# Kernel tuning notes

Measured on AMD Instinct MI355X. Metric: run time of the kernel, lower is better.

The kernel has to match this reference:

```python
import jax, jax.numpy as jnp
import numpy as np

C_IN = 144
PC = 288           # proj_channels = 2 * in_channels
HEADS = 12
DG = 12            # deformable groups
CLIP = 2
KH = KW = 3
A = KH * KW        # samples per clip per group (attention window 3x3)
PAD = 1
MAXMAG = 10.0
B, T, H, W = 1, 1, 64, 64


def _conv2d(x, w, b, pad):
    y = jax.lax.conv_general_dilated(x, w, (1, 1), [(pad, pad), (pad, pad)],
                                     dimension_numbers=('NCHW', 'OIHW', 'NCHW'))
    return y + b[None, :, None, None]


def _lrelu(x):
    return jnp.where(x >= 0, x, 0.1 * x)


def _linear_c(x, w, b):
    # per-pixel linear on channel dim; x: (..., Cin, h, w), w: (Cin, Cout)
    return jnp.einsum('...ihw,io->...ohw', x, w) + b[:, None, None]


def _bilinear_gather(feat, py, px):
    # feat: (b, clip, g, cg, h, w); py/px: (b, clip, g, A, h, w) absolute pixel coords
    # zero padding outside image (deformable-conv sampling semantics)
    b, cl, g, cg, h, w = feat.shape
    ff = feat.reshape(b, cl, g, cg, h * w)
    y0 = jnp.floor(py)
    x0 = jnp.floor(px)
    wy1 = py - y0
    wx1 = px - x0

    def corner(yc, xc, wt):
        valid = ((yc >= 0) & (yc < h) & (xc >= 0) & (xc < w)).astype(feat.dtype)
        yi = jnp.clip(yc, 0, h - 1).astype(jnp.int32)
        xi = jnp.clip(xc, 0, w - 1).astype(jnp.int32)
        idx = (yi * w + xi).reshape(b, cl, g, 1, -1)
        gat = jnp.take_along_axis(ff, idx, axis=-1).reshape(b, cl, g, cg, *py.shape[3:])
        return gat * (wt * valid)[:, :, :, None]

    out = corner(y0, x0, (1 - wy1) * (1 - wx1))
    out = out + corner(y0, x0 + 1, (1 - wy1) * wx1)
    out = out + corner(y0 + 1, x0, wy1 * (1 - wx1))
    out = out + corner(y0 + 1, x0 + 1, wy1 * wx1)
    return out  # (b, clip, g, cg, A, h, w)


def setup_inputs() -> dict:
    key = jax.random.key(0)
    ks = jax.random.split(key, 32)
    rn = lambda i, shp, s=1.0: jax.random.normal(ks[i], shp, dtype=jnp.float32) * s
    cin_off = C_IN * (1 + CLIP) + CLIP * 2   # 436
    c_off = CLIP * DG * A * 2                # 432
    d = {
        'q': rn(0, (B, T, C_IN, H, W)),
        'k': rn(1, (B, CLIP, C_IN, H, W)),
        'v': rn(2, (B, CLIP, C_IN, H, W)),
        'vpw0': rn(3, (B, T, C_IN, H, W)),
        'vpw1': rn(4, (B, T, C_IN, H, W)),
        'flow0': rn(5, (B, T, 2, H, W), 3.0),
        'flow1': rn(6, (B, T, 2, H, W), 3.0),
        'wo1': rn(7, (64, cin_off, 1, 1), 1.0 / np.sqrt(cin_off)),
        'bo1': rn(8, (64,), 0.01),
        'wo2': rn(9, (64, 64, 3, 3), 1.0 / np.sqrt(64 * 9)),
        'bo2': rn(10, (64,), 0.01),
        'wo3': rn(11, (64, 64, 3, 3), 1.0 / np.sqrt(64 * 9)),
        'bo3': rn(12, (64,), 0.01),
        'wo4': rn(13, (64, 64, 3, 3), 1.0 / np.sqrt(64 * 9)),
        'bo4': rn(14, (64,), 0.01),
        'wo5': rn(15, (64, 64, 3, 3), 1.0 / np.sqrt(64 * 9)),
        'bo5': rn(16, (64,), 0.01),
        'wo6': rn(17, (c_off, 64, 1, 1), 0.02),
        'bo6': rn(18, (c_off,), 0.01),
        'wq': rn(19, (C_IN, PC), 1.0 / np.sqrt(C_IN)),
        'bq': rn(20, (PC,), 0.01),
        'wk': rn(21, (C_IN, PC), 1.0 / np.sqrt(C_IN)),
        'bk': rn(22, (PC,), 0.01),
        'wv': rn(23, (C_IN, PC), 1.0 / np.sqrt(C_IN)),
        'bv': rn(24, (PC,), 0.01),
        'wp': rn(25, (PC, C_IN), 1.0 / np.sqrt(PC)),
        'bp': rn(26, (C_IN,), 0.01),
        'wm1': rn(27, (C_IN, 2 * C_IN), 1.0 / np.sqrt(C_IN)),
        'bm1': rn(28, (2 * C_IN,), 0.01),
        'wm2': rn(29, (2 * C_IN, C_IN), 1.0 / np.sqrt(2 * C_IN)),
        'bm2': rn(30, (C_IN,), 0.01),
    }
    return d


def reference(q, k, v, vpw0, vpw1, flow0, flow1,
              wo1, bo1, wo2, bo2, wo3, bo3, wo4, bo4, wo5, bo5, wo6, bo6,
              wq, bq, wk, bk, wv, bv, wp, bp, wm1, bm1, wm2, bm2):
    b, t, c, h, w = q.shape  # t == 1 here so q batch b*t matches kv batch b
    bt = b * t
    # --- offset predictor: Conv3d stack with time-kernel 1 == 2D convs ---
    x = jnp.concatenate([q, vpw0, vpw1, flow0, flow1], axis=2).reshape(bt, -1, h, w)
    x = _lrelu(_conv2d(x, wo1, bo1, 0))
    x = _lrelu(_conv2d(x, wo2, bo2, 1))
    x = _lrelu(_conv2d(x, wo3, bo3, 1))
    x = _lrelu(_conv2d(x, wo4, bo4, 1))
    x = _lrelu(_conv2d(x, wo5, bo5, 1))
    off = MAXMAG * jnp.tanh(_conv2d(x, wo6, bo6, 0))  # (bt, CLIP*DG*A*2, h, w)
    # add optical flow (channel-flipped to (y, x)) to every sample offset
    fyx = flow0.reshape(bt, 2, h, w)[:, ::-1]
    off = off + jnp.tile(fyx, (1, off.shape[1] // 2, 1, 1))
    off = off.reshape(bt, CLIP, DG, A, 2, h, w)
    ar = jnp.arange(A)
    by = (ar // KW - PAD).astype(q.dtype)  # kernel base offsets (stride=1, dil=1)
    bx = (ar % KW - PAD).astype(q.dtype)
    py = off[:, :, :, :, 0] + by[None, None, None, :, None, None] \
         + jnp.arange(h, dtype=q.dtype)[:, None]
    px = off[:, :, :, :, 1] + bx[None, None, None, :, None, None] \
         + jnp.arange(w, dtype=q.dtype)
    # --- q/k/v projections ---
    hd = PC // HEADS
    qp = _linear_c(q, wq, bq).reshape(bt, HEADS, hd, h, w)
    kp = _linear_c(k, wk, bk).reshape(b, CLIP, DG, PC // DG, h, w)
    vp = _linear_c(v, wv, bv).reshape(b, CLIP, DG, PC // DG, h, w)
    # --- deformable bilinear gather (per deformable group) ---
    ksamp = _bilinear_gather(kp, py, px).reshape(bt, CLIP, HEADS, hd, A, h, w)
    vsamp = _bilinear_gather(vp, py, px).reshape(bt, CLIP, HEADS, hd, A, h, w)
    # --- attention over CLIP*A sampled locations, per pixel per head ---
    scores = jnp.einsum('bmdyx,bcmdayx->bmcayx', qp, ksamp) * (hd ** -0.5)
    attn = jax.nn.softmax(scores.reshape(bt, HEADS, CLIP * A, h, w), axis=2)
    vflat = vsamp.transpose(0, 2, 1, 4, 3, 5, 6).reshape(bt, HEADS, CLIP * A, hd, h, w)
    out = jnp.einsum('bmsyx,bmsdyx->bmdyx', attn, vflat).reshape(b, t, PC, h, w)
    # --- output projection + MLP residual ---
    o = _linear_c(out, wp, bp)
    m = _linear_c(jax.nn.gelu(_linear_c(o, wm1, bm1), approximate=False), wm2, bm2)
    return o + m
```

## Files before the change

kernel.cpp:

```cpp
#include <hip/hip_runtime.h>
#include <hip/hip_bf16.h>
#include <math.h>

typedef __hip_bfloat16 bf16;
typedef __attribute__((ext_vector_type(8))) short bf16x8v;
typedef __attribute__((ext_vector_type(4))) float f32x4v;

#define NPIX 4096

__device__ __forceinline__ float b2f(bf16 v) { return __bfloat162float(v); }
__device__ __forceinline__ unsigned short f2bu(float f) {
    bf16 h = __float2bfloat16(f);
    return *(unsigned short*)&h;
}
__device__ __forceinline__ int detect_bf16(const unsigned short* __restrict__ qraw) {
    int lane = threadIdx.x & 63;
    unsigned short u = qraw[lane * 2];
    int e = (u >> 7) & 0xFF;
    unsigned long long ball = __ballot(e >= 100 && e <= 135);
    return __popcll(ball) > 32;
}
__device__ __forceinline__ float rdval(const void* s, int idx, int isbf) {
    return isbf ? b2f(((const bf16*)s)[idx]) : ((const float*)s)[idx];
}

#define OF_WO6 175680
#define OF_BO6 203328
#define OF_BO1 27904
#define OF_BO2 64832
#define OF_BO3 101760
#define OF_BO4 138688
#define OF_BO5 175616
#define OF_BQ  245232
#define OF_BK  286992
#define OF_BV  328752
#define OF_BP  370512
#define OF_BM1 412128
#define OF_BM2 453888
#define OF_FL0 454032

struct CArgs { const void* src[14]; int dstoff[14]; int n[14]; };
struct PPJob { const void* src; int dstS; int Mp, Kp, kr, mr, sstride, kind; };
struct PPArgs { PPJob j[11]; };

__global__ void misc_kernel(CArgs a, PPArgs pa, const void* __restrict__ q,
                            const void* __restrict__ k, const void* __restrict__ v,
                            const void* __restrict__ vp0, const void* __restrict__ vp1,
                            const void* __restrict__ fl0, const void* __restrict__ fl1,
                            float* __restrict__ cw, short* __restrict__ XS,
                            short* __restrict__ X1, short* __restrict__ wsS)
{
    const int isbf = detect_bf16((const unsigned short*)q);
    const int y = blockIdx.y;
    if (y < 14) {
        const int n = a.n[y];
        float* d = cw + a.dstoff[y];
        if (isbf) {
            const bf16* s = (const bf16*)a.src[y];
            for (int i = blockIdx.x * 256 + threadIdx.x; i < n; i += 256 * 16) d[i] = b2f(s[i]);
        } else {
            const float* s = (const float*)a.src[y];
            for (int i = blockIdx.x * 256 + threadIdx.x; i < n; i += 256 * 16) d[i] = s[i];
        }
    } else if (y < 24) {
        const int job = y - 14;
        const int z = job >> 1, half = job & 1;
        const int p = blockIdx.x * 256 + threadIdx.x;
        const void* srcs[5] = { q, k, k, v, v };
        const int clips[5] = { 0, 0, 1, 0, 1 };
        const size_t co = (size_t)clips[z] * 144 * NPIX;
        short* row = XS + (size_t)z * 655360 + (size_t)p * 160;
        for (int c0 = half * 72; c0 < half * 72 + 72; c0 += 8) {
            unsigned short h[8];
            if (isbf) {
                const bf16* s = (const bf16*)srcs[z] + co;
#pragma unroll
                for (int i = 0; i < 8; ++i) h[i] = f2bu(b2f(s[(size_t)(c0 + i) * NPIX + p]));
            } else {
                const float* s = (const float*)srcs[z] + co;
#pragma unroll
                for (int i = 0; i < 8; ++i) h[i] = f2bu(s[(size_t)(c0 + i) * NPIX + p]);
            }
            uint4 u;
            u.x = (unsigned)h[0] | ((unsigned)h[1] << 16);
            u.y = (unsigned)h[2] | ((unsigned)h[3] << 16);
            u.z = (unsigned)h[4] | ((unsigned)h[5] << 16);
            u.w = (unsigned)h[6] | ((unsigned)h[7] << 16);
            *(uint4*)(row + c0) = u;
        }
        if (half == 1) {
            uint4 zz; zz.x = zz.y = zz.z = zz.w = 0u;
            *(uint4*)(row + 144) = zz;
            *(uint4*)(row + 152) = zz;
        }
    } else if (y < 28) {
        const int sec = y - 24;
        const int p = blockIdx.x * 256 + threadIdx.x;
        short* row = X1 + (size_t)p * 448;
        if (sec < 3) {
            const void* srcs[3] = { q, vp0, vp1 };
            const int cbase = sec * 144;
            for (int c0 = 0; c0 < 144; c0 += 8) {
                unsigned short h[8];
                if (isbf) {
                    const bf16* s = (const bf16*)srcs[sec];
#pragma unroll
                    for (int i = 0; i < 8; ++i) h[i] = f2bu(b2f(s[(size_t)(c0 + i) * NPIX + p]));
                } else {
                    const float* s = (const float*)srcs[sec];
#pragma unroll
                    for (int i = 0; i < 8; ++i) h[i] = f2bu(s[(size_t)(c0 + i) * NPIX + p]);
                }
                uint4 u;
                u.x = (unsigned)h[0] | ((unsigned)h[1] << 16);
                u.y = (unsigned)h[2] | ((unsigned)h[3] << 16);
                u.z = (unsigned)h[4] | ((unsigned)h[5] << 16);
                u.w = (unsigned)h[6] | ((unsigned)h[7] << 16);
                *(uint4*)(row + cbase + c0) = u;
            }
        } else {
            unsigned short h[4];
            if (isbf) {
                const bf16* f0 = (const bf16*)fl0;
                const bf16* f1 = (const bf16*)fl1;
                h[0] = f2bu(b2f(f0[p]));
                h[1] = f2bu(b2f(f0[NPIX + p]));
                h[2] = f2bu(b2f(f1[p]));
                h[3] = f2bu(b2f(f1[NPIX + p]));
            } else {
                const float* f0 = (const float*)fl0;
                const float* f1 = (const float*)fl1;
                h[0] = f2bu(f0[p]);
                h[1] = f2bu(f0[NPIX + p]);
                h[2] = f2bu(f1[p]);
                h[3] = f2bu(f1[NPIX + p]);
            }
            uint4 u;
            u.x = (unsigned)h[0] | ((unsigned)h[1] << 16);
            u.y = (unsigned)h[2] | ((unsigned)h[3] << 16);
            u.z = 0u; u.w = 0u;
            *(uint4*)(row + 432) = u;
            uint4 zz; zz.x = zz.y = zz.z = zz.w = 0u;
            *(uint4*)(row + 440) = zz;
        }
    } else {
        PPJob J = pa.j[y - 28];
        const int tot = J.Mp * J.Kp;
        for (int e = blockIdx.x * 256 + threadIdx.x; e < tot; e += 256 * 16) {
            int m = e / J.Kp, kk = e - m * J.Kp;
            float vv = 0.f;
            if (J.kind == 0) { if (kk < J.kr) vv = rdval(J.src, m * J.sstride + kk, isbf); }
            else if (J.kind == 1) { if (kk < J.kr && m < J.mr) vv = rdval(J.src, kk * J.sstride + m, isbf); }
            else { int c = kk & 63, tap = kk >> 6; if (kk < J.kr) vv = rdval(J.src, m * J.sstride + c * 9 + tap, isbf); }
            wsS[J.dstS + e] = (short)f2bu(vv);
        }
    }
}

struct GemmDesc {
    const short* A; const short* B; const float* bias;
    void* dst; void* dst2; const unsigned short* qraw;
    int Mp, Mreal, mode, gofs, ostride, obase, nwaves;
};
struct GemmDesc5 { GemmDesc d[5]; };

template <int TM, int TN, int BM, int KP>
__global__ __launch_bounds__(256) void gemm_kernel(GemmDesc5 gd)
{
    const GemmDesc d = gd.d[blockIdx.z];
    const int wid = blockIdx.x * 4 + (threadIdx.x >> 6);
    if (wid >= d.nwaves) return;
    const int lane = threadIdx.x & 63;
    const int tiles_m = d.Mp / (16 * TM);
    const int m0 = (wid % tiles_m) * (16 * TM);
    const int p0 = (wid / tiles_m) * (16 * TN);
    const int ar = lane & 15;
    const int kq = (lane >> 4) * 8;

    f32x4v acc[TM][TN];
#pragma unroll
    for (int i = 0; i < TM; ++i)
#pragma unroll
        for (int j = 0; j < TN; ++j) acc[i][j] = (f32x4v){0.f, 0.f, 0.f, 0.f};

#pragma unroll
    for (int k0 = 0; k0 < KP; k0 += 32) {
        bf16x8v a[TM], b[TN];
#pragma unroll
        for (int i = 0; i < TM; ++i)
            a[i] = *(const bf16x8v*)(d.A + (size_t)(m0 + i * 16 + ar) * KP + k0 + kq);
        if (BM == 0) {
#pragma unroll
            for (int j = 0; j < TN; ++j)
                b[j] = *(const bf16x8v*)(d.B + (size_t)(p0 + j * 16 + ar) * KP + k0 + kq);
        } else {
            const int tap = k0 >> 6;
            const int cc = (k0 & 63) + kq;
            const int dy = tap / 3 - 1, dx = tap % 3 - 1;
#pragma unroll
            for (int j = 0; j < TN; ++j) {
                const int pix = p0 + j * 16 + ar;
                const int yy = (pix >> 6) + dy, xx = (pix & 63) + dx;
                const bool ok = ((unsigned)yy < 64u) & ((unsigned)xx < 64u);
                const int np = min(max(yy, 0), 63) * 64 + min(max(xx, 0), 63);
                bf16x8v bv = *(const bf16x8v*)(d.B + (size_t)np * 64 + cc);
                if (!ok) bv = (bf16x8v)(short)0;
                b[j] = bv;
            }
        }
#pragma unroll
        for (int i = 0; i < TM; ++i)
#pragma unroll
            for (int j = 0; j < TN; ++j)
                acc[i][j] = __builtin_amdgcn_mfma_f32_16x16x32_bf16(a[i], b[j], acc[i][j], 0, 0, 0);
    }

    const int isbf = (d.mode == 5) ? detect_bf16(d.qraw) : 0;
#pragma unroll
    for (int i = 0; i < TM; ++i) {
#pragma unroll
        for (int j = 0; j < TN; ++j) {
            const int pcol = p0 + j * 16 + (lane & 15);
            const int mb = m0 + i * 16 + (lane >> 4) * 4;
            float vv[4];
#pragma unroll
            for (int r = 0; r < 4; ++r) {
                const int m = mb + r;
                vv[r] = acc[i][j][r];
                if (m < d.Mreal) vv[r] += d.bias[m];
            }
            if (d.mode == 0) {
#pragma unroll
                for (int r = 0; r < 4; ++r) vv[r] = (vv[r] >= 0.f) ? vv[r] : 0.1f * vv[r];
                uint2 u;
                u.x = (unsigned)f2bu(vv[0]) | ((unsigned)f2bu(vv[1]) << 16);
                u.y = (unsigned)f2bu(vv[2]) | ((unsigned)f2bu(vv[3]) << 16);
                *(uint2*)((unsigned short*)d.dst + (size_t)pcol * d.Mp + mb) = u;
            } else if (d.mode == 1) {
                const int g = mb / 24 + d.gofs;
                uint2 u;
                u.x = (unsigned)f2bu(vv[0]) | ((unsigned)f2bu(vv[1]) << 16);
                u.y = (unsigned)f2bu(vv[2]) | ((unsigned)f2bu(vv[3]) << 16);
                *(uint2*)((unsigned short*)d.dst +
                          ((size_t)g * NPIX + pcol) * d.ostride + (mb % 24) + d.obase) = u;
            } else if (d.mode == 3) {
                uint2 u;
                u.x = (unsigned)f2bu(vv[0]) | ((unsigned)f2bu(vv[1]) << 16);
                u.y = (unsigned)f2bu(vv[2]) | ((unsigned)f2bu(vv[3]) << 16);
                *(uint2*)((unsigned short*)d.dst + (size_t)pcol * 160 + mb) = u;
                if (mb < 144)
                    *(float4*)((float*)d.dst2 + (size_t)pcol * 144 + mb) =
                        make_float4(vv[0], vv[1], vv[2], vv[3]);
            } else if (d.mode == 4) {
#pragma unroll
                for (int r = 0; r < 4; ++r)
                    vv[r] = 0.5f * vv[r] * (1.f + erff(vv[r] * 0.70710678118654752f));
                uint2 u;
                u.x = (unsigned)f2bu(vv[0]) | ((unsigned)f2bu(vv[1]) << 16);
                u.y = (unsigned)f2bu(vv[2]) | ((unsigned)f2bu(vv[3]) << 16);
                *(uint2*)((unsigned short*)d.dst + (size_t)pcol * d.Mp + mb) = u;
            } else {
#pragma unroll
                for (int r = 0; r < 4; ++r) {
                    const int m = mb + r;
                    if (m < 144) {
                        float v = vv[r] + ((float*)d.dst2)[(size_t)pcol * 144 + m];
                        if (isbf) ((unsigned short*)d.dst)[(size_t)m * NPIX + pcol] = f2bu(v);
                        else      ((float*)d.dst)[(size_t)m * NPIX + pcol] = v;
                    }
                }
            }
        }
    }
}

__global__ __launch_bounds__(256) void conv6_kernel(const short* __restrict__ YF,
                                                    const float* __restrict__ cw,
                                                    float* __restrict__ py, float* __restrict__ px)
{
    const int p = blockIdx.x * 256 + threadIdx.x;
    const int o0 = blockIdx.y * 16;
    const uint4* yrow = (const uint4*)(YF + (size_t)p * 64);
    const float* wb = cw + OF_WO6 + o0 * 64;

    float acc[16];
#pragma unroll
    for (int j = 0; j < 16; ++j) acc[j] = cw[OF_BO6 + o0 + j];

#pragma unroll
    for (int c = 0; c < 8; ++c) {
        uint4 u = yrow[c];
        float a0 = __uint_as_float(u.x << 16);
        float a1 = __uint_as_float(u.x & 0xFFFF0000u);
        float a2 = __uint_as_float(u.y << 16);
        float a3 = __uint_as_float(u.y & 0xFFFF0000u);
        float a4 = __uint_as_float(u.z << 16);
        float a5 = __uint_as_float(u.z & 0xFFFF0000u);
        float a6 = __uint_as_float(u.w << 16);
        float a7 = __uint_as_float(u.w & 0xFFFF0000u);
#pragma unroll
        for (int j = 0; j < 16; ++j) {
            const float* wr = wb + j * 64 + c * 8;
            acc[j] += a0 * wr[0] + a1 * wr[1] + a2 * wr[2] + a3 * wr[3]
                    + a4 * wr[4] + a5 * wr[5] + a6 * wr[6] + a7 * wr[7];
        }
    }

    const float f_y = cw[OF_FL0 + NPIX + p];
    const float f_x = cw[OF_FL0 + p];
    const float yf = (float)(p >> 6), xf = (float)(p & 63);
#pragma unroll
    for (int j = 0; j < 16; ++j) {
        int o = o0 + j;
        float val = 10.f * tanhf(acc[j]);
        int s = o >> 1;
        int a_idx = s % 9;
        if ((o & 1) == 0) py[s * NPIX + p] = val + f_y + (float)(a_idx / 3 - 1) + yf;
        else              px[s * NPIX + p] = val + f_x + (float)(a_idx % 3 - 1) + xf;
    }
}

__device__ __forceinline__ float dot12(const bf16* __restrict__ row, const float* qv) {
    const uint2* s = (const uint2*)row;
    float d = 0.f;
#pragma unroll
    for (int c = 0; c < 3; ++c) {
        uint2 u = s[c];
        d += qv[c * 4 + 0] * __uint_as_float(u.x << 16);
        d += qv[c * 4 + 1] * __uint_as_float(u.x & 0xFFFF0000u);
        d += qv[c * 4 + 2] * __uint_as_float(u.y << 16);
        d += qv[c * 4 + 3] * __uint_as_float(u.y & 0xFFFF0000u);
    }
    return d;
}
__device__ __forceinline__ void acc12(float* ov, const bf16* __restrict__ row, float f) {
    const uint2* s = (const uint2*)row;
#pragma unroll
    for (int c = 0; c < 3; ++c) {
        uint2 u = s[c];
        ov[c * 4 + 0] += f * __uint_as_float(u.x << 16);
        ov[c * 4 + 1] += f * __uint_as_float(u.x & 0xFFFF0000u);
        ov[c * 4 + 2] += f * __uint_as_float(u.y << 16);
        ov[c * 4 + 3] += f * __uint_as_float(u.y & 0xFFFF0000u);
    }
}

__global__ __launch_bounds__(256) void attn_kernel(
    const bf16* __restrict__ qp, const bf16* __restrict__ kv,
    const float* __restrict__ py, const float* __restrict__ px,
    unsigned short* __restrict__ att)
{
    const int t = blockIdx.x * 256 + threadIdx.x;
    const int ch = t & 1;
    const int clip = (t >> 1) & 1;
    const int sh = (t >> 2) & 1;
    const int pp = t >> 3;
    const int m = pp >> 12;
    const int p = pp & 4095;

    float qv[12];
    {
        const uint2* s = (const uint2*)(qp + (size_t)(m * 4096 + p) * 24 + ch * 12);
#pragma unroll
        for (int c = 0; c < 3; ++c) {
            uint2 u = s[c];
            qv[c * 4 + 0] = __uint_as_float(u.x << 16);
            qv[c * 4 + 1] = __uint_as_float(u.x & 0xFFFF0000u);
            qv[c * 4 + 2] = __uint_as_float(u.y << 16);
            qv[c * 4 + 3] = __uint_as_float(u.y & 0xFFFF0000u);
        }
    }

    const int gidx = clip * 12 + m;
    const bf16* kvb = kv + (size_t)gidx * 4096 * 48 + ch * 12;
    const int sbase = gidx * 9;
    const int a0 = sh ? 5 : 0;
    const int na = sh ? 4 : 5;

    float mxL = -1e30f, sumL = 0.f;
    float ov[12];
#pragma unroll
    for (int j = 0; j < 12; ++j) ov[j] = 0.f;

    for (int i = 0; i < na; ++i) {
        const int a = a0 + i;
        const float fy = py[(sbase + a) * NPIX + p];
        const float fx = px[(sbase + a) * NPIX + p];
        const float y0f = floorf(fy), x0f = floorf(fx);
        const float wy = fy - y0f, wx = fx - x0f;
        const int iy = (int)y0f, ix = (int)x0f;
        const float vy0 = ((unsigned)iy < 64u) ? 1.f : 0.f;
        const float vy1 = ((unsigned)(iy + 1) < 64u) ? 1.f : 0.f;
        const float vx0 = ((unsigned)ix < 64u) ? 1.f : 0.f;
        const float vx1 = ((unsigned)(ix + 1) < 64u) ? 1.f : 0.f;
        const int iy0 = min(max(iy, 0), 63), iy1 = min(max(iy + 1, 0), 63);
        const int ix0 = min(max(ix, 0), 63), ix1 = min(max(ix + 1, 0), 63);
        const float w0 = (1.f - wy) * (1.f - wx) * vy0 * vx0;
        const float w1 = (1.f - wy) * wx * vy0 * vx1;
        const float w2 = wy * (1.f - wx) * vy1 * vx0;
        const float w3 = wy * wx * vy1 * vx1;
        const int n0 = iy0 * 64 + ix0, n1 = iy0 * 64 + ix1;
        const int n2 = iy1 * 64 + ix0, n3 = iy1 * 64 + ix1;
        float part = w0 * dot12(kvb + (size_t)n0 * 48, qv)
                   + w1 * dot12(kvb + (size_t)n1 * 48, qv)
                   + w2 * dot12(kvb + (size_t)n2 * 48, qv)
                   + w3 * dot12(kvb + (size_t)n3 * 48, qv);
        float full = part + __shfl_xor(part, 1, 64);
        float e = full * 0.20412414523193154f;
        float newmx = fmaxf(mxL, e);
        float r = __expf(mxL - newmx);
        float ee = __expf(e - newmx);
        mxL = newmx;
        sumL = sumL * r + ee;
#pragma unroll
        for (int j = 0; j < 12; ++j) ov[j] *= r;
        acc12(ov, kvb + (size_t)n0 * 48 + 24, ee * w0);
        acc12(ov, kvb + (size_t)n1 * 48 + 24, ee * w1);
        acc12(ov, kvb + (size_t)n2 * 48 + 24, ee * w2);
        acc12(ov, kvb + (size_t)n3 * 48 + 24, ee * w3);
    }

    float M = fmaxf(mxL, __shfl_xor(mxL, 4, 64));
    M = fmaxf(M, __shfl_xor(M, 2, 64));
    const float sc = __expf(mxL - M);
    float s = sumL * sc;
    s += __shfl_xor(s, 4, 64);
    s += __shfl_xor(s, 2, 64);
    const float inv = 1.f / s;
#pragma unroll
    for (int j = 0; j < 12; ++j) {
        float v = ov[j] * sc;
        v += __shfl_xor(v, 4, 64);
        v += __shfl_xor(v, 2, 64);
        ov[j] = v * inv;
    }
    if (clip == 0 && sh == 0) {
        unsigned short* ab = att + (size_t)p * 288 + m * 24 + ch * 12;
#pragma unroll
        for (int c = 0; c < 3; ++c) {
            uint2 u;
            u.x = (unsigned)f2bu(ov[c * 4 + 0]) | ((unsigned)f2bu(ov[c * 4 + 1]) << 16);
            u.y = (unsigned)f2bu(ov[c * 4 + 2]) | ((unsigned)f2bu(ov[c * 4 + 3]) << 16);
            ((uint2*)ab)[c] = u;
        }
    }
}

__global__ void diag_kernel(float* __restrict__ out, int n, float v)
{
    int i = blockIdx.x * 256 + threadIdx.x;
    if (i < n) out[i] = (i == 0 ? v : 0.f);
}

extern "C" void kernel_launch(void* const* d_in, const int* in_sizes, int n_in,
                              void* d_out, int out_size, void* d_ws, size_t ws_size,
                              hipStream_t stream)
{
    const size_t REQUIRED = 75000000;
    if (ws_size < REQUIRED) {
        float code = 1000.0f + (float)(ws_size >> 20);
        diag_kernel<<<dim3((out_size + 255) / 256), 256, 0, stream>>>((float*)d_out, out_size, code);
        return;
    }

    char* W = (char*)d_ws;
    short* wsS = (short*)W;
    float* cw = (float*)(W + 64);

    short* conv1w = wsS + 1000000;
    short* conv3w[4] = { wsS + 1028672, wsS + 1065536, wsS + 1102400, wsS + 1139264 };
    short* wqb = wsS + 1176128, *wkb = wsS + 1222208, *wvb = wsS + 1268288;
    short* wpS = wsS + 1314368, *wm1S = wsS + 1360448, *wm2S = wsS + 1406528;

    short* XS = (short*)(W + 16777216);
    short* X1 = (short*)(W + 25165824);
    bf16*  QP = (bf16*)(W + 33554432);
    bf16*  KV = (bf16*)(W + 36700160);
    short* Y0 = (short*)(W + 50331648);
    short* Y1 = (short*)(W + 50855936);
    short* YF = (short*)(W + 51380224);
    float* PY = (float*)(W + 54525952);
    float* PX = (float*)(W + 58064896);
    unsigned short* ATT = (unsigned short*)(W + 62914560);
    short* OPM = (short*)(W + 67108864);
    float* O32 = (float*)(W + 68419584);
    short* M1  = (short*)(W + 71303168);

    const unsigned short* qraw = (const unsigned short*)d_in[0];

    CArgs ca;
    const int srcidx[14] = {8,10,12,14,16,17,18,20,22,24,26,28,30,5};
    const int dsto[14]   = {OF_BO1,OF_BO2,OF_BO3,OF_BO4,OF_BO5,OF_WO6,OF_BO6,
                            OF_BQ,OF_BK,OF_BV,OF_BP,OF_BM1,OF_BM2,OF_FL0};
    for (int i = 0; i < 14; ++i) {
        ca.src[i] = d_in[srcidx[i]];
        ca.dstoff[i] = dsto[i];
        ca.n[i] = in_sizes[srcidx[i]];
    }
    PPArgs pp;
    pp.j[0]  = { d_in[7],  1000000, 64, 448, 436, 64,  436, 0 };
    pp.j[1]  = { d_in[9],  1028672, 64, 576, 576, 64,  576, 2 };
    pp.j[2]  = { d_in[11], 1065536, 64, 576, 576, 64,  576, 2 };
    pp.j[3]  = { d_in[13], 1102400, 64, 576, 576, 64,  576, 2 };
    pp.j[4]  = { d_in[15], 1139264, 64, 576, 576, 64,  576, 2 };
    pp.j[5]  = { d_in[19], 1176128, 288, 160, 144, 288, 288, 1 };
    pp.j[6]  = { d_in[21], 1222208, 288, 160, 144, 288, 288, 1 };
    pp.j[7]  = { d_in[23], 1268288, 288, 160, 144, 288, 288, 1 };
    pp.j[8]  = { d_in[25], 1314368, 160, 288, 288, 144, 144, 1 };
    pp.j[9]  = { d_in[27], 1360448, 288, 160, 144, 288, 288, 1 };
    pp.j[10] = { d_in[29], 1406528, 160, 288, 288, 144, 144, 1 };
    misc_kernel<<<dim3(16, 39), 256, 0, stream>>>(ca, pp, d_in[0], d_in[1], d_in[2], d_in[3],
                                                  d_in[4], d_in[5], d_in[6], cw, XS, X1, wsS);

    GemmDesc5 g3;
    const short* Xz[5] = { XS, XS + 655360, XS + 1310720, XS + 1966080, XS + 2621440 };
    const short* Az[5] = { wqb, wkb, wkb, wvb, wvb };
    const float* Bz[5] = { cw + OF_BQ, cw + OF_BK, cw + OF_BK, cw + OF_BV, cw + OF_BV };
    bf16* Dz[5] = { QP, KV, KV, KV, KV };
    const int Gz[5] = { 0, 0, 12, 0, 12 };
    const int Oz[5] = { 24, 48, 48, 48, 48 };
    const int Bo[5] = { 0, 0, 0, 24, 24 };
    for (int z = 0; z < 5; ++z)
        g3.d[z] = { Az[z], Xz[z], Bz[z], Dz[z], nullptr, qraw, 288, 288, 1, Gz[z], Oz[z], Bo[z], 1152 };
    gemm_kernel<2, 2, 0, 160><<<dim3(288, 1, 5), 256, 0, stream>>>(g3);

    GemmDesc5 g1;
    g1.d[0] = { conv1w, X1, cw + OF_BO1, Y0, nullptr, qraw, 64, 64, 0, 0, 0, 0, 1024 };
    gemm_kernel<1, 1, 0, 448><<<dim3(256, 1, 1), 256, 0, stream>>>(g1);

    const float* cb[4] = { cw + OF_BO2, cw + OF_BO3, cw + OF_BO4, cw + OF_BO5 };
    short* cin[4] = { Y0, Y1, Y0, Y1 };
    short* coutp[4] = { Y1, Y0, Y1, YF };
    for (int i = 0; i < 4; ++i) {
        GemmDesc5 gc;
        gc.d[0] = { conv3w[i], cin[i], cb[i], coutp[i], nullptr, qraw, 64, 64, 0, 0, 0, 0, 1024 };
        gemm_kernel<1, 1, 1, 576><<<dim3(256, 1, 1), 256, 0, stream>>>(gc);
    }

    conv6_kernel<<<dim3(16, 27), 256, 0, stream>>>(YF, cw, PY, PX);

    attn_kernel<<<dim3(1536), 256, 0, stream>>>(QP, KV, PY, PX, ATT);

    GemmDesc5 gwp;
    gwp.d[0] = { wpS, (const short*)ATT, cw + OF_BP, OPM, O32, qraw, 160, 144, 3, 0, 0, 0, 640 };
    gemm_kernel<2, 2, 0, 288><<<dim3(160, 1, 1), 256, 0, stream>>>(gwp);

    GemmDesc5 gm1;
    gm1.d[0] = { wm1S, OPM, cw + OF_BM1, M1, nullptr, qraw, 288, 288, 4, 0, 0, 0, 1152 };
    gemm_kernel<2, 2, 0, 160><<<dim3(288, 1, 1), 256, 0, stream>>>(gm1);

    GemmDesc5 gm2;
    gm2.d[0] = { wm2S, M1, cw + OF_BM2, d_out, O32, qraw, 160, 144, 5, 0, 0, 0, 640 };
    gemm_kernel<2, 2, 0, 288><<<dim3(160, 1, 1), 256, 0, stream>>>(gm2);
}
```

Baseline: 287.8 us.

## Interleave sampling coords and use two-pass softmax with skipped out-of-bounds corners

The conv6 kernel now writes the y/x sampling coordinates interleaved as float2, and the attention kernel reads them with one vector load. The online softmax is replaced by a two-pass scheme: all scores are computed first, the max and sum are reduced across lanes, and then the values are accumulated with normalized weights. This removes the per-step rescale of the accumulator and its extra exponentials. Corner gathers that fall outside the image are now skipped by branch instead of being clamped and multiplied by zero, at the cost of recomputing the bilinear weights in the second pass and some divergence.

```diff
diff --git a/kernel.cpp b/kernel.cpp
--- a/kernel.cpp
+++ b/kernel.cpp
@@ -276,7 +276,7 @@
 
 __global__ __launch_bounds__(256) void conv6_kernel(const short* __restrict__ YF,
                                                     const float* __restrict__ cw,
-                                                    float* __restrict__ py, float* __restrict__ px)
+                                                    float* __restrict__ pyx)
 {
     const int p = blockIdx.x * 256 + threadIdx.x;
     const int o0 = blockIdx.y * 16;
@@ -310,13 +310,15 @@
     const float f_x = cw[OF_FL0 + p];
     const float yf = (float)(p >> 6), xf = (float)(p & 63);
 #pragma unroll
-    for (int j = 0; j < 16; ++j) {
-        int o = o0 + j;
-        float val = 10.f * tanhf(acc[j]);
-        int s = o >> 1;
-        int a_idx = s % 9;
-        if ((o & 1) == 0) py[s * NPIX + p] = val + f_y + (float)(a_idx / 3 - 1) + yf;
-        else              px[s * NPIX + p] = val + f_x + (float)(a_idx % 3 - 1) + xf;
+    for (int j = 0; j < 16; j += 2) {
+        const int s = (o0 + j) >> 1;
+        const int a_idx = s % 9;
+        float vy = 10.f * tanhf(acc[j]);
+        float vx = 10.f * tanhf(acc[j + 1]);
+        float2 o;
+        o.x = vy + f_y + (float)(a_idx / 3 - 1) + yf;
+        o.y = vx + f_x + (float)(a_idx % 3 - 1) + xf;
+        *(float2*)(pyx + 2 * ((size_t)s * NPIX + p)) = o;
     }
 }
 
@@ -347,8 +349,7 @@
 
 __global__ __launch_bounds__(256) void attn_kernel(
     const bf16* __restrict__ qp, const bf16* __restrict__ kv,
-    const float* __restrict__ py, const float* __restrict__ px,
-    unsigned short* __restrict__ att)
+    const float* __restrict__ pyx, unsigned short* __restrict__ att)
 {
     const int t = blockIdx.x * 256 + threadIdx.x;
     const int ch = t & 1;
@@ -377,62 +378,76 @@
     const int a0 = sh ? 5 : 0;
     const int na = sh ? 4 : 5;
 
-    float mxL = -1e30f, sumL = 0.f;
+    float e[5], fyv[5], fxv[5];
+    float mx = -1e30f;
+#pragma unroll
+    for (int i = 0; i < 5; ++i) {
+        e[i] = -1e30f; fyv[i] = 0.f; fxv[i] = 0.f;
+        if (i < na) {
+            const int a = a0 + i;
+            const float2 f2v = *(const float2*)(pyx + 2 * ((size_t)(sbase + a) * NPIX + p));
+            const float fy = f2v.x, fx = f2v.y;
+            fyv[i] = fy; fxv[i] = fx;
+            const float y0 = floorf(fy), x0 = floorf(fx);
+            const float wy = fy - y0, wx = fx - x0;
+            const int iy = (int)y0, ix = (int)x0;
+            const float w00 = (1.f - wy) * (1.f - wx), w01 = (1.f - wy) * wx;
+            const float w10 = wy * (1.f - wx), w11 = wy * wx;
+            float part = 0.f;
+            if ((unsigned)iy < 64u) {
+                const bf16* rr = kvb + (size_t)(iy * 64) * 48;
+                if ((unsigned)ix < 64u)       part += w00 * dot12(rr + ix * 48, qv);
+                if ((unsigned)(ix + 1) < 64u) part += w01 * dot12(rr + (ix + 1) * 48, qv);
+            }
+            if ((unsigned)(iy + 1) < 64u) {
+                const bf16* rr = kvb + (size_t)((iy + 1) * 64) * 48;
+                if ((unsigned)ix < 64u)       part += w10 * dot12(rr + ix * 48, qv);
+                if ((unsigned)(ix + 1) < 64u) part += w11 * dot12(rr + (ix + 1) * 48, qv);
+            }
+            float full = part + __shfl_xor(part, 1, 64);
+            e[i] = full * 0.20412414523193154f;
+            mx = fmaxf(mx, e[i]);
+        }
+    }
+    mx = fmaxf(mx, __shfl_xor(mx, 4, 64));
+    mx = fmaxf(mx, __shfl_xor(mx, 2, 64));
+    float sum = 0.f;
+#pragma unroll
+    for (int i = 0; i < 5; ++i) {
+        if (i < na) { e[i] = __expf(e[i] - mx); sum += e[i]; }
+    }
+    sum += __shfl_xor(sum, 4, 64);
+    sum += __shfl_xor(sum, 2, 64);
+    const float inv = 1.f / sum;
+
     float ov[12];
 #pragma unroll
     for (int j = 0; j < 12; ++j) ov[j] = 0.f;
 
-    for (int i = 0; i < na; ++i) {
-        const int a = a0 + i;
-        const float fy = py[(sbase + a) * NPIX + p];
-        const float fx = px[(sbase + a) * NPIX + p];
-        const float y0f = floorf(fy), x0f = floorf(fx);
-        const float wy = fy - y0f, wx = fx - x0f;
-        const int iy = (int)y0f, ix = (int)x0f;
-        const float vy0 = ((unsigned)iy < 64u) ? 1.f : 0.f;
-        const float vy1 = ((unsigned)(iy + 1) < 64u) ? 1.f : 0.f;
-        const float vx0 = ((unsigned)ix < 64u) ? 1.f : 0.f;
-        const float vx1 = ((unsigned)(ix + 1) < 64u) ? 1.f : 0.f;
-        const int iy0 = min(max(iy, 0), 63), iy1 = min(max(iy + 1, 0), 63);
-        const int ix0 = min(max(ix, 0), 63), ix1 = min(max(ix + 1, 0), 63);
-        const float w0 = (1.f - wy) * (1.f - wx) * vy0 * vx0;
-        const float w1 = (1.f - wy) * wx * vy0 * vx1;
-        const float w2 = wy * (1.f - wx) * vy1 * vx0;
-        const float w3 = wy * wx * vy1 * vx1;
-        const int n0 = iy0 * 64 + ix0, n1 = iy0 * 64 + ix1;
-        const int n2 = iy1 * 64 + ix0, n3 = iy1 * 64 + ix1;
-        float part = w0 * dot12(kvb + (size_t)n0 * 48, qv)
-                   + w1 * dot12(kvb + (size_t)n1 * 48, qv)
-                   + w2 * dot12(kvb + (size_t)n2 * 48, qv)
-                   + w3 * dot12(kvb + (size_t)n3 * 48, qv);
-        float full = part + __shfl_xor(part, 1, 64);
-        float e = full * 0.20412414523193154f;
-        float newmx = fmaxf(mxL, e);
-        float r = __expf(mxL - newmx);
-        float ee = __expf(e - newmx);
-        mxL = newmx;
-        sumL = sumL * r + ee;
-#pragma unroll
-        for (int j = 0; j < 12; ++j) ov[j] *= r;
-        acc12(ov, kvb + (size_t)n0 * 48 + 24, ee * w0);
-        acc12(ov, kvb + (size_t)n1 * 48 + 24, ee * w1);
-        acc12(ov, kvb + (size_t)n2 * 48 + 24, ee * w2);
-        acc12(ov, kvb + (size_t)n3 * 48 + 24, ee * w3);
-    }
-
-    float M = fmaxf(mxL, __shfl_xor(mxL, 4, 64));
-    M = fmaxf(M, __shfl_xor(M, 2, 64));
-    const float sc = __expf(mxL - M);
-    float s = sumL * sc;
-    s += __shfl_xor(s, 4, 64);
-    s += __shfl_xor(s, 2, 64);
-    const float inv = 1.f / s;
+#pragma unroll
+    for (int i = 0; i < 5; ++i) {
+        if (i < na) {
+            const float wa = e[i] * inv;
+            const float fy = fyv[i], fx = fxv[i];
+            const float y0 = floorf(fy), x0 = floorf(fx);
+            const float wy = fy - y0, wx = fx - x0;
+            const int iy = (int)y0, ix = (int)x0;
+            if ((unsigned)iy < 64u) {
+                const bf16* rr = kvb + (size_t)(iy * 64) * 48 + 24;
+                if ((unsigned)ix < 64u)       acc12(ov, rr + ix * 48, wa * (1.f - wy) * (1.f - wx));
+                if ((unsigned)(ix + 1) < 64u) acc12(ov, rr + (ix + 1) * 48, wa * (1.f - wy) * wx);
+            }
+            if ((unsigned)(iy + 1) < 64u) {
+                const bf16* rr = kvb + (size_t)((iy + 1) * 64) * 48 + 24;
+                if ((unsigned)ix < 64u)       acc12(ov, rr + ix * 48, wa * wy * (1.f - wx));
+                if ((unsigned)(ix + 1) < 64u) acc12(ov, rr + (ix + 1) * 48, wa * wy * wx);
+            }
+        }
+    }
 #pragma unroll
     for (int j = 0; j < 12; ++j) {
-        float v = ov[j] * sc;
-        v += __shfl_xor(v, 4, 64);
-        v += __shfl_xor(v, 2, 64);
-        ov[j] = v * inv;
+        ov[j] += __shfl_xor(ov[j], 4, 64);
+        ov[j] += __shfl_xor(ov[j], 2, 64);
     }
     if (clip == 0 && sh == 0) {
         unsigned short* ab = att + (size_t)p * 288 + m * 24 + ch * 12;
@@ -479,8 +494,7 @@
     short* Y0 = (short*)(W + 50331648);
     short* Y1 = (short*)(W + 50855936);
     short* YF = (short*)(W + 51380224);
-    float* PY = (float*)(W + 54525952);
-    float* PX = (float*)(W + 58064896);
+    float* PYX = (float*)(W + 54525952);
     unsigned short* ATT = (unsigned short*)(W + 62914560);
     short* OPM = (short*)(W + 67108864);
     float* O32 = (float*)(W + 68419584);
@@ -537,9 +551,9 @@
         gemm_kernel<1, 1, 1, 576><<<dim3(256, 1, 1), 256, 0, stream>>>(gc);
     }
 
-    conv6_kernel<<<dim3(16, 27), 256, 0, stream>>>(YF, cw, PY, PX);
-
-    attn_kernel<<<dim3(1536), 256, 0, stream>>>(QP, KV, PY, PX, ATT);
+    conv6_kernel<<<dim3(16, 27), 256, 0, stream>>>(YF, cw, PYX);
+
+    attn_kernel<<<dim3(1536), 256, 0, stream>>>(QP, KV, PYX, ATT);
 
     GemmDesc5 gwp;
     gwp.d[0] = { wpS, (const short*)ATT, cw + OF_BP, OPM, O32, qraw, 160, 144, 3, 0, 0, 0, 640 };
```

After: 285.8 us. Within noise of the previous version (-0.7%).
